# Kernel tuning notes

Measured on AMD Instinct MI355X. Metric: run time of the kernel, lower is better.

Reference implementation:

```python
import jax, jax.numpy as jnp
import numpy as np

HID = 64   # RNN_HID_SIZE
FEAT = 9   # feature dim, hard-coded in module
T = 36     # SEQ_LEN


def setup_inputs() -> dict:
    key = jax.random.key(0)
    ks = jax.random.split(key, 20)
    B = 16384

    def u(k, shape, stdv):
        return jax.random.uniform(k, shape, jnp.float32, -stdv, stdv)

    s_h = 1.0 / np.sqrt(HID)    # stdv for layers with 64 rows / fan-in 64
    s_f = 1.0 / np.sqrt(FEAT)   # stdv 1/3 for feature-sized layers
    s_c = 1.0 / np.sqrt(2 * FEAT)  # weight_combine: Linear(18, 9)

    inp = {
        "values": jax.random.normal(ks[0], (B, T, FEAT), jnp.float32),
        "masks": (jax.random.uniform(ks[1], (B, T, FEAT)) < 0.8).astype(jnp.float32),
        "deltas": jax.random.uniform(ks[2], (B, T, FEAT), jnp.float32, 0.0, 5.0),
        # TemporalDecay h: W [64, 9], stdv = 1/sqrt(64)
        "W_gh": u(ks[3], (HID, FEAT), s_h), "b_gh": u(ks[4], (HID,), s_h),
        # TemporalDecay x (diag): W [9, 9], stdv = 1/sqrt(9)
        "W_gx": u(ks[5], (FEAT, FEAT), s_f), "b_gx": u(ks[6], (FEAT,), s_f),
        # hist_reg: Linear(64, 9)
        "W_hist": u(ks[7], (FEAT, HID), s_h), "b_hist": u(ks[8], (FEAT,), s_h),
        "W_feat": u(ks[9], (FEAT, FEAT), s_f), "b_feat": u(ks[10], (FEAT,), s_f),
        # weight_combine: Linear(18, 9)
        "W_comb": u(ks[11], (FEAT, 2 * FEAT), s_c), "b_comb": u(ks[12], (FEAT,), s_c),
        # LSTMCell(18, 64): gates order i, f, g, o
        "W_ih": u(ks[13], (4 * HID, 2 * FEAT), s_h), "W_hh": u(ks[14], (4 * HID, HID), s_h),
        "b_ih": u(ks[15], (4 * HID,), s_h), "b_hh": u(ks[16], (4 * HID,), s_h),
    }
    return inp


def reference(values, masks, deltas, W_gh, b_gh, W_gx, b_gx, W_hist, b_hist,
              W_feat, b_feat, W_comb, b_comb, W_ih, W_hh, b_ih, b_hh):
    B = values.shape[0]
    dt = values.dtype
    eye = jnp.eye(FEAT, dtype=dt)
    Wgx_diag = W_gx * eye            # TemporalDecay diag mask
    Wfeat_off = W_feat * (1.0 - eye)

    # time-major for scan: [T, B, F]
    xs = (jnp.swapaxes(values, 0, 1), jnp.swapaxes(masks, 0, 1), jnp.swapaxes(deltas, 0, 1))

    def step(carry, xt):
        h, c, loss = carry
        x, m, d = xt
        gamma_h = jnp.exp(-jax.nn.relu(d @ W_gh.T + b_gh))   # [B, 64]
        gamma_x = jnp.exp(-jax.nn.relu(d @ Wgx_diag.T + b_gx))  # [B, 9]
        h = h * gamma_h
        x_h = h @ W_hist.T + b_hist
        denom = jnp.sum(m) + 1e-5
        x_c = m * x + (1.0 - m) * x_h
        z_h = x_c @ Wfeat_off.T + b_feat
        alpha = jnp.concatenate([gamma_x, m], axis=1) @ W_comb.T + b_comb
        c_h = alpha * z_h + (1.0 - alpha) * x_h
        loss = loss + (jnp.sum(jnp.abs(x - x_h) * m)
                       + jnp.sum(jnp.abs(x - z_h) * m)
                       + jnp.sum(jnp.abs(x - c_h) * m)) / denom
        c_c = m * x + (1.0 - m) * c_h
        inp = jnp.concatenate([c_c, m], axis=1)              # [B, 18]
        gates = inp @ W_ih.T + b_ih + h @ W_hh.T + b_hh      # [B, 256]
        i, f, g, o = jnp.split(gates, 4, axis=1)
        c = jax.nn.sigmoid(f) * c + jax.nn.sigmoid(i) * jnp.tanh(g)
        h = jax.nn.sigmoid(o) * jnp.tanh(c)
        return (h, c, loss), c_c

    init = (jnp.zeros((B, HID), dt), jnp.zeros((B, HID), dt), jnp.zeros((), dt))
    (_, _, loss), imps = jax.lax.scan(step, init, xs)
    imputations = jnp.swapaxes(imps, 0, 1)  # [B, T, F]
    return loss / T, imputations
```

## Files before the change

### kernel.cpp

```cpp
#include <hip/hip_runtime.h>

typedef _Float16 hh;
typedef _Float16 h2  __attribute__((ext_vector_type(2)));
typedef _Float16 v4h __attribute__((ext_vector_type(4)));
typedef _Float16 v8h __attribute__((ext_vector_type(8)));
typedef float v4f    __attribute__((ext_vector_type(4)));
typedef unsigned short u16;

#define T_STEPS 36
#define FEAT 9
#define HID 64
#define BT 32
#define SIN_STR 232
#define PK_STR 40

__device__ __forceinline__ float fast_exp2(float x) {
#if __has_builtin(__builtin_amdgcn_exp2f)
  return __builtin_amdgcn_exp2f(x);
#else
  return exp2f(x);
#endif
}
__device__ __forceinline__ float fast_rcp(float x) {
#if __has_builtin(__builtin_amdgcn_rcpf)
  return __builtin_amdgcn_rcpf(x);
#else
  return 1.f / x;
#endif
}
__device__ __forceinline__ float sigmoid_fast(float x) {
  return fast_rcp(1.f + fast_exp2(x * -1.442695041f));
}
__device__ __forceinline__ float tanh_fast(float x) {
  return 1.f - 2.f * fast_rcp(1.f + fast_exp2(x * 2.885390082f));
}
__device__ __forceinline__ float fdot2(h2 a, h2 b, float c) {
#if __has_builtin(__builtin_amdgcn_fdot2)
  return __builtin_amdgcn_fdot2(a, b, c, false);
#else
  return c + (float)a[0] * (float)b[0] + (float)a[1] * (float)b[1];
#endif
}
__device__ __forceinline__ h2 mkh2(hh a, hh b) { h2 r; r[0] = a; r[1] = b; return r; }
__device__ __forceinline__ v4f mfma16(v8h a, v8h b, v4f c) {
  return __builtin_amdgcn_mfma_f32_16x16x32_f16(a, b, c, 0, 0, 0);
}

__global__ void zero_ws(float* __restrict__ ws, float* __restrict__ out) {
  int tid = threadIdx.x;
  if (tid < T_STEPS) ws[tid] = 0.f;
  if (tid == 0) out[0] = 0.f;
}

__global__ __launch_bounds__(256) void denom_kernel(const float* __restrict__ masks,
                                                    float* __restrict__ ws) {
  __shared__ float red[T_STEPS];
  const int tid = threadIdx.x;
  const int e = blockIdx.x * 256 + tid;
  if (tid < T_STEPS) red[tid] = 0.f;
  float acc[T_STEPS];
#pragma unroll
  for (int t = 0; t < T_STEPS; ++t) acc[t] = 0.f;
  const float4* p = (const float4*)masks + (size_t)e * 81;
#pragma unroll
  for (int c = 0; c < 81; ++c) {
    float4 v = p[c];
    acc[(4 * c) / 9]     += v.x;
    acc[(4 * c + 1) / 9] += v.y;
    acc[(4 * c + 2) / 9] += v.z;
    acc[(4 * c + 3) / 9] += v.w;
  }
  __syncthreads();
  int rot = tid % T_STEPS;
#pragma unroll
  for (int t = 0; t < T_STEPS; ++t) {
    int tt = rot + t; if (tt >= T_STEPS) tt -= T_STEPS;
    atomicAdd(&red[tt], acc[tt]);
  }
  __syncthreads();
  if (tid < T_STEPS) atomicAdd(&ws[tid], red[tid]);
}


__global__ __launch_bounds__(256, 2) void rits_kernel(
    const float* __restrict__ values, const float* __restrict__ masks,
    const float* __restrict__ deltas,
    const float* __restrict__ W_gh, const float* __restrict__ b_gh,
    const float* __restrict__ W_gx, const float* __restrict__ b_gx,
    const float* __restrict__ W_hist, const float* __restrict__ b_hist,
    const float* __restrict__ W_feat, const float* __restrict__ b_feat,
    const float* __restrict__ W_comb, const float* __restrict__ b_comb,
    const float* __restrict__ W_ih, const float* __restrict__ W_hh,
    const float* __restrict__ b_ih, const float* __restrict__ b_hh,
    const float* __restrict__ denom, float* __restrict__ out) {

  __shared__ __align__(16) hh sIn[BT * SIN_STR];
  __shared__ __align__(16) hh sPk[BT * PK_STR];
  __shared__ float sRed[256];

  const int tid = threadIdx.x;
  const int lane = tid & 63;
  const int wid = tid >> 6;
  const int q = lane >> 4;
  const int nlo = lane & 15;
  const int b0 = blockIdx.x * BT;
  const int j_col = 16 * wid + nlo;

  v8h bG[4][3];
#pragma unroll
  for (int p = 0; p < 4; ++p)
#pragma unroll
    for (int kt = 0; kt < 3; ++kt) {
      int n = 64 * p + j_col;
      v8h r;
#pragma unroll
      for (int jj = 0; jj < 8; ++jj) {
        int k = kt * 32 + q * 8 + jj;
        float v = 0.f;
        if (k < 18)       v = W_ih[n * 18 + k];
        else if (k < 82)  v = W_hh[n * 64 + (k - 18)];
        else if (k == 82) v = b_ih[n] + b_hh[n];
        r[jj] = (hh)v;
      }
      bG[p][kt] = r;
    }
  v8h bH[3];
#pragma unroll
  for (int kt = 0; kt < 3; ++kt) {
    v8h r;
#pragma unroll
    for (int jj = 0; jj < 8; ++jj) {
      int k = kt * 32 + q * 8 + jj;
      float v = 0.f;
      if (nlo < 9) {
        if (k >= 18 && k < 82) v = W_hist[nlo * 64 + (k - 18)];
        else if (k == 82)      v = b_hist[nlo];
      }
      r[jj] = (hh)v;
    }
    bH[kt] = r;
  }
  v8h bGamA, bGamB;
  {
    int n = j_col;
    v8h ra, rb;
#pragma unroll
    for (int jj = 0; jj < 8; ++jj) {
      int k = q * 8 + jj;
      float va = 0.f, vb = 0.f;
      if (k == 2) va = b_gh[n];
      else if (k >= 16 && k < 25) va = W_gh[n * 9 + (k - 16)];
      if (k >= 2 && k < 11) vb = W_gh[n * 9 + (k - 2)];
      else if (k == 12) vb = b_gh[n];
      ra[jj] = (hh)va; rb[jj] = (hh)vb;
    }
    bGamA = ra; bGamB = rb;
  }

  const int eP = tid >> 3, fqw = tid & 7;
  h2 wf1[5], wf2[5], wc1[9], wc2[9];
  float bf1 = b_feat[fqw], bf2 = b_feat[8];
  float bc1v = b_comb[fqw], bc2v = b_comb[8];
#pragma unroll
  for (int j = 0; j < 5; ++j) {
    int i0 = 2 * j, i1 = 2 * j + 1;
    hh a0 = (hh)((i0 == fqw) ? 0.f : W_feat[fqw * 9 + i0]);
    hh a1 = (hh)((i1 < 9) ? ((i1 == fqw) ? 0.f : W_feat[fqw * 9 + i1]) : 0.f);
    wf1[j] = mkh2(a0, a1);
    hh c0 = (hh)((i0 == 8) ? 0.f : W_feat[8 * 9 + i0]);
    hh c1 = (hh)((i1 < 9) ? W_feat[8 * 9 + i1] : 0.f);
    wf2[j] = mkh2(c0, c1);
  }
#pragma unroll
  for (int j = 0; j < 9; ++j) {
    wc1[j] = mkh2((hh)W_comb[fqw * 18 + 2 * j], (hh)W_comb[fqw * 18 + 2 * j + 1]);
    wc2[j] = mkh2((hh)W_comb[8 * 18 + 2 * j], (hh)W_comb[8 * 18 + 2 * j + 1]);
  }
  float wgx[9], bgxv[9];
#pragma unroll
  for (int f = 0; f < 9; ++f) { wgx[f] = W_gx[f * 9 + f]; bgxv[f] = b_gx[f]; }

  for (int i = tid; i < BT * SIN_STR; i += 256) sIn[i] = (hh)0.f;
  __syncthreads();
  if (tid < BT) {
    sIn[tid * SIN_STR + 82] = (hh)1.f;
    sIn[tid * SIN_STR + 178] = (hh)1.f;
    sIn[tid * SIN_STR + 212] = (hh)1.f;
  }
  const int e1 = tid / 9, f1 = tid - 9 * e1;
  const int e2g = (tid + 256) / 9, f2g = (tid + 256) - 9 * e2g;
  float dreg0 = 0.f, dreg1 = 0.f;
  {
    size_t off = (size_t)(b0 + e1) * (T_STEPS * FEAT) + f1;
    sPk[e1 * PK_STR + f1] = (hh)values[off];
    sPk[e1 * PK_STR + 9 + f1] = (hh)masks[off];
    sPk[e1 * PK_STR + 27 + f1] = (hh)deltas[off];
    float d1 = deltas[off + FEAT];
    dreg0 = d1;
    sIn[e1 * SIN_STR + 202 + f1] = (hh)d1;
    if (tid < 32) {
      size_t off2 = (size_t)(b0 + e2g) * (T_STEPS * FEAT) + f2g;
      sPk[e2g * PK_STR + f2g] = (hh)values[off2];
      sPk[e2g * PK_STR + 9 + f2g] = (hh)masks[off2];
      sPk[e2g * PK_STR + 27 + f2g] = (hh)deltas[off2];
      float d1b = deltas[off2 + FEAT];
      dreg1 = d1b;
      sIn[e2g * SIN_STR + 202 + f2g] = (hh)d1b;
    }
  }
  __syncthreads();

  float c_s[8];
#pragma unroll
  for (int i = 0; i < 8; ++i) c_s[i] = 0.f;
  float loss_acc = 0.f;

  for (int t = 0; t < T_STEPS; ++t) {
    const float inv_den = fast_rcp(denom[t] + 1e-5f);

    v4f gacc[2];
    {
      const int sel = (t + 1) & 1;
      const int awin = 176 + sel * 24;
#pragma unroll
      for (int mt = 0; mt < 2; ++mt) {
        v8h a = *(const v8h*)&sIn[(mt * 16 + nlo) * SIN_STR + awin + q * 8];
        v4f z4 = {0.f, 0.f, 0.f, 0.f};
        gacc[mt] = sel ? mfma16(a, bGamB, z4) : mfma16(a, bGamA, z4);
      }
    }
    if (wid < 2) {
      const int base = (t & 1) * 96;
      v4f acc = {0.f, 0.f, 0.f, 0.f};
#pragma unroll
      for (int kt = 0; kt < 3; ++kt) {
        v8h a = *(const v8h*)&sIn[(wid * 16 + nlo) * SIN_STR + base + kt * 32 + q * 8];
        acc = mfma16(a, bH[kt], acc);
      }
      if (nlo < 9) {
#pragma unroll
        for (int r = 0; r < 4; ++r)
          sPk[(wid * 16 + q * 4 + r) * PK_STR + 18 + nlo] = (hh)acc[r];
      }
    }
    __syncthreads();

    {
      const int pk = eP * PK_STR;
      float x_f  = (float)sPk[pk + fqw];
      float m_f  = (float)sPk[pk + 9 + fqw];
      float xh_f = (float)sPk[pk + 18 + fqw];
      v8h r0 = *(const v8h*)&sPk[pk];
      v8h r1 = *(const v8h*)&sPk[pk + 8];
      v8h r2 = *(const v8h*)&sPk[pk + 16];
      v8h r3 = *(const v8h*)&sPk[pk + 24];
      v4h r4 = *(const v4h*)&sPk[pk + 32];
      hh xxh[9] = {r0[0],r0[1],r0[2],r0[3],r0[4],r0[5],r0[6],r0[7],r1[0]};
      hh mmh[9] = {r1[1],r1[2],r1[3],r1[4],r1[5],r1[6],r1[7],r2[0],r2[1]};
      hh xhh[9] = {r2[2],r2[3],r2[4],r2[5],r2[6],r2[7],r3[0],r3[1],r3[2]};
      hh ddh[9] = {r3[3],r3[4],r3[5],r3[6],r3[7],r4[0],r4[1],r4[2],r4[3]};
      hh xch[10];
#pragma unroll
      for (int f = 0; f < 9; ++f) {
        u16 mb = __builtin_bit_cast(u16, mmh[f]);
        xch[f] = mb ? xxh[f] : xhh[f];
      }
      xch[9] = (hh)0.f;
      hh gxh[9];
#pragma unroll
      for (int f = 0; f < 9; ++f) {
        float y = fmaxf((float)ddh[f] * wgx[f] + bgxv[f], 0.f);
        gxh[f] = (hh)fast_exp2(y * -1.442695041f);
      }
      h2 xc2[5] = {mkh2(xch[0],xch[1]), mkh2(xch[2],xch[3]), mkh2(xch[4],xch[5]),
                   mkh2(xch[6],xch[7]), mkh2(xch[8],xch[9])};
      h2 g2[9]  = {mkh2(gxh[0],gxh[1]), mkh2(gxh[2],gxh[3]), mkh2(gxh[4],gxh[5]),
                   mkh2(gxh[6],gxh[7]), mkh2(gxh[8],mmh[0]), mkh2(mmh[1],mmh[2]),
                   mkh2(mmh[3],mmh[4]), mkh2(mmh[5],mmh[6]), mkh2(mmh[7],mmh[8])};
      float z1 = bf1, a1 = bc1v;
#pragma unroll
      for (int j = 0; j < 5; ++j) z1 = fdot2(wf1[j], xc2[j], z1);
#pragma unroll
      for (int j = 0; j < 9; ++j) a1 = fdot2(wc1[j], g2[j], a1);
      float ch1 = xh_f + a1 * (z1 - xh_f);
      bool obs1 = (m_f != 0.f);
      float cc1 = obs1 ? x_f : ch1;
      float lterm = obs1 ? (fabsf(x_f - xh_f) + fabsf(x_f - z1) + fabsf(x_f - ch1)) : 0.f;
      const int pb = (t & 1) * 96;
      sIn[eP * SIN_STR + pb + fqw] = (hh)cc1;
      sIn[eP * SIN_STR + pb + 9 + fqw] = (hh)m_f;
      out[1 + (size_t)(b0 + eP) * (T_STEPS * FEAT) + t * FEAT + fqw] = cc1;
      if (fqw == 7) {
        float z2 = bf2, a2 = bc2v;
#pragma unroll
        for (int j = 0; j < 5; ++j) z2 = fdot2(wf2[j], xc2[j], z2);
#pragma unroll
        for (int j = 0; j < 9; ++j) a2 = fdot2(wc2[j], g2[j], a2);
        float x8 = (float)xxh[8], m8 = (float)mmh[8], xh8 = (float)xhh[8];
        float ch2 = xh8 + a2 * (z2 - xh8);
        bool obs2 = (m8 != 0.f);
        float cc2 = obs2 ? x8 : ch2;
        lterm += obs2 ? (fabsf(x8 - xh8) + fabsf(x8 - z2) + fabsf(x8 - ch2)) : 0.f;
        sIn[eP * SIN_STR + pb + 8] = (hh)cc2;
        sIn[eP * SIN_STR + pb + 17] = mmh[8];
        out[1 + (size_t)(b0 + eP) * (T_STEPS * FEAT) + t * FEAT + 8] = cc2;
      }
      loss_acc += lterm * inv_den;
    }
    __syncthreads();

    {
      float px0 = 0.f, pm0 = 0.f, px1 = 0.f, pm1 = 0.f, pd0 = 0.f, pd1 = 0.f;
      const bool pre1 = (t + 1 < T_STEPS), pre2 = (t + 2 < T_STEPS);
      if (pre1) {
        size_t off = (size_t)(b0 + e1) * (T_STEPS * FEAT) + (t + 1) * FEAT + f1;
        px0 = values[off]; pm0 = masks[off];
        if (tid < 32) {
          size_t off2 = (size_t)(b0 + e2g) * (T_STEPS * FEAT) + (t + 1) * FEAT + f2g;
          px1 = values[off2]; pm1 = masks[off2];
        }
      }
      if (pre2) {
        size_t offd = (size_t)(b0 + e1) * (T_STEPS * FEAT) + (t + 2) * FEAT + f1;
        pd0 = deltas[offd];
        if (tid < 32) {
          size_t offd2 = (size_t)(b0 + e2g) * (T_STEPS * FEAT) + (t + 2) * FEAT + f2g;
          pd1 = deltas[offd2];
        }
      }

      const int base = (t & 1) * 96;
      const int pub = ((t + 1) & 1) * 96;
      v8h af[2][3];
#pragma unroll
      for (int mt = 0; mt < 2; ++mt)
#pragma unroll
        for (int kt = 0; kt < 3; ++kt)
          af[mt][kt] = *(const v8h*)&sIn[(mt * 16 + nlo) * SIN_STR + base + kt * 32 + q * 8];

      v4f acc[2][4];
#pragma unroll
      for (int mt = 0; mt < 2; ++mt)
#pragma unroll
        for (int p = 0; p < 4; ++p)
          acc[mt][p] = (v4f){0.f, 0.f, 0.f, 0.f};
#pragma unroll
      for (int mt = 0; mt < 2; ++mt)
#pragma unroll
        for (int p = 0; p < 4; ++p)
#pragma unroll
          for (int kt = 0; kt < 3; ++kt)
            acc[mt][p] = mfma16(af[mt][kt], bG[p][kt], acc[mt][p]);

#pragma unroll
      for (int mt = 0; mt < 2; ++mt) {
#pragma unroll
        for (int r = 0; r < 4; ++r) {
          float ig = sigmoid_fast(acc[mt][0][r]);
          float fg = sigmoid_fast(acc[mt][1][r]);
          float gg = tanh_fast(acc[mt][2][r]);
          float og = sigmoid_fast(acc[mt][3][r]);
          float cn = fg * c_s[mt * 4 + r] + ig * gg;
          c_s[mt * 4 + r] = cn;
          float hn = og * tanh_fast(cn);
          float gam = fast_exp2(fmaxf(gacc[mt][r], 0.f) * -1.442695041f);
          sIn[(mt * 16 + q * 4 + r) * SIN_STR + pub + 18 + j_col] = (hh)(hn * gam);
        }
      }

      if (pre1) {
        sPk[e1 * PK_STR + f1] = (hh)px0;
        sPk[e1 * PK_STR + 9 + f1] = (hh)pm0;
        sPk[e1 * PK_STR + 27 + f1] = (hh)dreg0;
        if (tid < 32) {
          sPk[e2g * PK_STR + f2g] = (hh)px1;
          sPk[e2g * PK_STR + 9 + f2g] = (hh)pm1;
          sPk[e2g * PK_STR + 27 + f2g] = (hh)dreg1;
        }
      }
      if (pre2) {
        const int sb = 192 + (t & 1) * 10;
        sIn[e1 * SIN_STR + sb + f1] = (hh)pd0;
        dreg0 = pd0;
        if (tid < 32) { sIn[e2g * SIN_STR + sb + f2g] = (hh)pd1; dreg1 = pd1; }
      }
    }
    __syncthreads();
  }

  sRed[tid] = loss_acc;
  __syncthreads();
  for (int k = 128; k > 0; k >>= 1) {
    if (tid < k) sRed[tid] += sRed[tid + k];
    __syncthreads();
  }
  if (tid == 0) atomicAdd(out, sRed[0] * (1.f / (float)T_STEPS));
}

extern "C" void kernel_launch(void* const* d_in, const int* in_sizes, int n_in,
                              void* d_out, int out_size, void* d_ws, size_t ws_size,
                              hipStream_t stream) {
  const float* values = (const float*)d_in[0];
  const float* masks  = (const float*)d_in[1];
  const float* deltas = (const float*)d_in[2];
  const float* W_gh   = (const float*)d_in[3];
  const float* b_gh   = (const float*)d_in[4];
  const float* W_gx   = (const float*)d_in[5];
  const float* b_gx   = (const float*)d_in[6];
  const float* W_hist = (const float*)d_in[7];
  const float* b_hist = (const float*)d_in[8];
  const float* W_feat = (const float*)d_in[9];
  const float* b_feat = (const float*)d_in[10];
  const float* W_comb = (const float*)d_in[11];
  const float* b_comb = (const float*)d_in[12];
  const float* W_ih   = (const float*)d_in[13];
  const float* W_hh   = (const float*)d_in[14];
  const float* b_ih   = (const float*)d_in[15];
  const float* b_hh   = (const float*)d_in[16];

  float* out = (float*)d_out;
  float* ws  = (float*)d_ws;
  int B = in_sizes[0] / (T_STEPS * FEAT);

  zero_ws<<<1, 64, 0, stream>>>(ws, out);
  denom_kernel<<<B / 256, 256, 0, stream>>>(masks, ws);
  rits_kernel<<<B / BT, 256, 0, stream>>>(values, masks, deltas,
                                          W_gh, b_gh, W_gx, b_gx,
                                          W_hist, b_hist, W_feat, b_feat,
                                          W_comb, b_comb, W_ih, W_hh,
                                          b_ih, b_hh, ws, out);
}
```

Baseline: 284.4 us.

## Halve batch tile per block to raise occupancy and re-split mask denominator reduction

After: 496.2 us. 74.5% more time.

```diff
diff --git a/kernel.cpp b/kernel.cpp
--- a/kernel.cpp
+++ b/kernel.cpp
@@ -10,7 +10,7 @@
 #define T_STEPS 36
 #define FEAT 9
 #define HID 64
-#define BT 32
+#define BT 16
 #define SIN_STR 232
 #define PK_STR 40
 
@@ -56,33 +56,27 @@
                                                     float* __restrict__ ws) {
   __shared__ float red[T_STEPS];
   const int tid = threadIdx.x;
-  const int e = blockIdx.x * 256 + tid;
   if (tid < T_STEPS) red[tid] = 0.f;
-  float acc[T_STEPS];
-#pragma unroll
-  for (int t = 0; t < T_STEPS; ++t) acc[t] = 0.f;
-  const float4* p = (const float4*)masks + (size_t)e * 81;
-#pragma unroll
-  for (int c = 0; c < 81; ++c) {
+  __syncthreads();
+  const int idx = blockIdx.x * 256 + tid;
+  const int t0 = (idx % 9) * 4;
+  const float4* p = (const float4*)masks + (size_t)idx * 9;
+  float acc[4] = {0.f, 0.f, 0.f, 0.f};
+#pragma unroll
+  for (int c = 0; c < 9; ++c) {
     float4 v = p[c];
     acc[(4 * c) / 9]     += v.x;
     acc[(4 * c + 1) / 9] += v.y;
     acc[(4 * c + 2) / 9] += v.z;
     acc[(4 * c + 3) / 9] += v.w;
   }
-  __syncthreads();
-  int rot = tid % T_STEPS;
-#pragma unroll
-  for (int t = 0; t < T_STEPS; ++t) {
-    int tt = rot + t; if (tt >= T_STEPS) tt -= T_STEPS;
-    atomicAdd(&red[tt], acc[tt]);
-  }
+#pragma unroll
+  for (int j = 0; j < 4; ++j) atomicAdd(&red[t0 + j], acc[j]);
   __syncthreads();
   if (tid < T_STEPS) atomicAdd(&ws[tid], red[tid]);
 }
 
-
-__global__ __launch_bounds__(256, 2) void rits_kernel(
+__global__ __launch_bounds__(256, 4) void rits_kernel(
     const float* __restrict__ values, const float* __restrict__ masks,
     const float* __restrict__ deltas,
     const float* __restrict__ W_gh, const float* __restrict__ b_gh,
@@ -188,9 +182,9 @@
     sIn[tid * SIN_STR + 212] = (hh)1.f;
   }
   const int e1 = tid / 9, f1 = tid - 9 * e1;
-  const int e2g = (tid + 256) / 9, f2g = (tid + 256) - 9 * e2g;
-  float dreg0 = 0.f, dreg1 = 0.f;
-  {
+  const bool ldr = (tid < 9 * BT);
+  float dreg0 = 0.f;
+  if (ldr) {
     size_t off = (size_t)(b0 + e1) * (T_STEPS * FEAT) + f1;
     sPk[e1 * PK_STR + f1] = (hh)values[off];
     sPk[e1 * PK_STR + 9 + f1] = (hh)masks[off];
@@ -198,54 +192,42 @@
     float d1 = deltas[off + FEAT];
     dreg0 = d1;
     sIn[e1 * SIN_STR + 202 + f1] = (hh)d1;
-    if (tid < 32) {
-      size_t off2 = (size_t)(b0 + e2g) * (T_STEPS * FEAT) + f2g;
-      sPk[e2g * PK_STR + f2g] = (hh)values[off2];
-      sPk[e2g * PK_STR + 9 + f2g] = (hh)masks[off2];
-      sPk[e2g * PK_STR + 27 + f2g] = (hh)deltas[off2];
-      float d1b = deltas[off2 + FEAT];
-      dreg1 = d1b;
-      sIn[e2g * SIN_STR + 202 + f2g] = (hh)d1b;
-    }
-  }
-  __syncthreads();
-
-  float c_s[8];
-#pragma unroll
-  for (int i = 0; i < 8; ++i) c_s[i] = 0.f;
+  }
+  __syncthreads();
+
+  float c_s[4];
+#pragma unroll
+  for (int i = 0; i < 4; ++i) c_s[i] = 0.f;
   float loss_acc = 0.f;
 
   for (int t = 0; t < T_STEPS; ++t) {
     const float inv_den = fast_rcp(denom[t] + 1e-5f);
 
-    v4f gacc[2];
+    v4f gacc;
     {
       const int sel = (t + 1) & 1;
       const int awin = 176 + sel * 24;
-#pragma unroll
-      for (int mt = 0; mt < 2; ++mt) {
-        v8h a = *(const v8h*)&sIn[(mt * 16 + nlo) * SIN_STR + awin + q * 8];
-        v4f z4 = {0.f, 0.f, 0.f, 0.f};
-        gacc[mt] = sel ? mfma16(a, bGamB, z4) : mfma16(a, bGamA, z4);
-      }
-    }
-    if (wid < 2) {
+      v8h a = *(const v8h*)&sIn[nlo * SIN_STR + awin + q * 8];
+      v4f z4 = {0.f, 0.f, 0.f, 0.f};
+      gacc = sel ? mfma16(a, bGamB, z4) : mfma16(a, bGamA, z4);
+    }
+    if (wid == 0) {
       const int base = (t & 1) * 96;
       v4f acc = {0.f, 0.f, 0.f, 0.f};
 #pragma unroll
       for (int kt = 0; kt < 3; ++kt) {
-        v8h a = *(const v8h*)&sIn[(wid * 16 + nlo) * SIN_STR + base + kt * 32 + q * 8];
+        v8h a = *(const v8h*)&sIn[nlo * SIN_STR + base + kt * 32 + q * 8];
         acc = mfma16(a, bH[kt], acc);
       }
       if (nlo < 9) {
 #pragma unroll
         for (int r = 0; r < 4; ++r)
-          sPk[(wid * 16 + q * 4 + r) * PK_STR + 18 + nlo] = (hh)acc[r];
+          sPk[(q * 4 + r) * PK_STR + 18 + nlo] = (hh)acc[r];
       }
     }
     __syncthreads();
 
-    {
+    if (eP < BT) {
       const int pk = eP * PK_STR;
       float x_f  = (float)sPk[pk + fqw];
       float m_f  = (float)sPk[pk + 9 + fqw];
@@ -310,79 +292,57 @@
     __syncthreads();
 
     {
-      float px0 = 0.f, pm0 = 0.f, px1 = 0.f, pm1 = 0.f, pd0 = 0.f, pd1 = 0.f;
-      const bool pre1 = (t + 1 < T_STEPS), pre2 = (t + 2 < T_STEPS);
+      float px0 = 0.f, pm0 = 0.f, pd0 = 0.f;
+      const bool pre1 = ldr && (t + 1 < T_STEPS);
+      const bool pre2 = ldr && (t + 2 < T_STEPS);
       if (pre1) {
         size_t off = (size_t)(b0 + e1) * (T_STEPS * FEAT) + (t + 1) * FEAT + f1;
         px0 = values[off]; pm0 = masks[off];
-        if (tid < 32) {
-          size_t off2 = (size_t)(b0 + e2g) * (T_STEPS * FEAT) + (t + 1) * FEAT + f2g;
-          px1 = values[off2]; pm1 = masks[off2];
-        }
       }
       if (pre2) {
         size_t offd = (size_t)(b0 + e1) * (T_STEPS * FEAT) + (t + 2) * FEAT + f1;
         pd0 = deltas[offd];
-        if (tid < 32) {
-          size_t offd2 = (size_t)(b0 + e2g) * (T_STEPS * FEAT) + (t + 2) * FEAT + f2g;
-          pd1 = deltas[offd2];
-        }
       }
 
       const int base = (t & 1) * 96;
       const int pub = ((t + 1) & 1) * 96;
-      v8h af[2][3];
-#pragma unroll
-      for (int mt = 0; mt < 2; ++mt)
+      v8h af[3];
+#pragma unroll
+      for (int kt = 0; kt < 3; ++kt)
+        af[kt] = *(const v8h*)&sIn[nlo * SIN_STR + base + kt * 32 + q * 8];
+
+      v4f acc[4];
+#pragma unroll
+      for (int p = 0; p < 4; ++p)
+        acc[p] = (v4f){0.f, 0.f, 0.f, 0.f};
+#pragma unroll
+      for (int p = 0; p < 4; ++p)
 #pragma unroll
         for (int kt = 0; kt < 3; ++kt)
-          af[mt][kt] = *(const v8h*)&sIn[(mt * 16 + nlo) * SIN_STR + base + kt * 32 + q * 8];
-
-      v4f acc[2][4];
-#pragma unroll
-      for (int mt = 0; mt < 2; ++mt)
-#pragma unroll
-        for (int p = 0; p < 4; ++p)
-          acc[mt][p] = (v4f){0.f, 0.f, 0.f, 0.f};
-#pragma unroll
-      for (int mt = 0; mt < 2; ++mt)
-#pragma unroll
-        for (int p = 0; p < 4; ++p)
-#pragma unroll
-          for (int kt = 0; kt < 3; ++kt)
-            acc[mt][p] = mfma16(af[mt][kt], bG[p][kt], acc[mt][p]);
-
-#pragma unroll
-      for (int mt = 0; mt < 2; ++mt) {
-#pragma unroll
-        for (int r = 0; r < 4; ++r) {
-          float ig = sigmoid_fast(acc[mt][0][r]);
-          float fg = sigmoid_fast(acc[mt][1][r]);
-          float gg = tanh_fast(acc[mt][2][r]);
-          float og = sigmoid_fast(acc[mt][3][r]);
-          float cn = fg * c_s[mt * 4 + r] + ig * gg;
-          c_s[mt * 4 + r] = cn;
-          float hn = og * tanh_fast(cn);
-          float gam = fast_exp2(fmaxf(gacc[mt][r], 0.f) * -1.442695041f);
-          sIn[(mt * 16 + q * 4 + r) * SIN_STR + pub + 18 + j_col] = (hh)(hn * gam);
-        }
+          acc[p] = mfma16(af[kt], bG[p][kt], acc[p]);
+
+#pragma unroll
+      for (int r = 0; r < 4; ++r) {
+        float ig = sigmoid_fast(acc[0][r]);
+        float fg = sigmoid_fast(acc[1][r]);
+        float gg = tanh_fast(acc[2][r]);
+        float og = sigmoid_fast(acc[3][r]);
+        float cn = fg * c_s[r] + ig * gg;
+        c_s[r] = cn;
+        float hn = og * tanh_fast(cn);
+        float gam = fast_exp2(fmaxf(gacc[r], 0.f) * -1.442695041f);
+        sIn[(q * 4 + r) * SIN_STR + pub + 18 + j_col] = (hh)(hn * gam);
       }
 
       if (pre1) {
         sPk[e1 * PK_STR + f1] = (hh)px0;
         sPk[e1 * PK_STR + 9 + f1] = (hh)pm0;
         sPk[e1 * PK_STR + 27 + f1] = (hh)dreg0;
-        if (tid < 32) {
-          sPk[e2g * PK_STR + f2g] = (hh)px1;
-          sPk[e2g * PK_STR + 9 + f2g] = (hh)pm1;
-          sPk[e2g * PK_STR + 27 + f2g] = (hh)dreg1;
-        }
       }
       if (pre2) {
         const int sb = 192 + (t & 1) * 10;
         sIn[e1 * SIN_STR + sb + f1] = (hh)pd0;
         dreg0 = pd0;
-        if (tid < 32) { sIn[e2g * SIN_STR + sb + f2g] = (hh)pd1; dreg1 = pd1; }
       }
     }
     __syncthreads();
@@ -423,7 +383,7 @@
   int B = in_sizes[0] / (T_STEPS * FEAT);
 
   zero_ws<<<1, 64, 0, stream>>>(ws, out);
-  denom_kernel<<<B / 256, 256, 0, stream>>>(masks, ws);
+  denom_kernel<<<(B * 9) / 256, 256, 0, stream>>>(masks, ws);
   rits_kernel<<<B / BT, 256, 0, stream>>>(values, masks, deltas,
                                           W_gh, b_gh, W_gx, b_gx,
                                           W_hist, b_hist, W_feat, b_feat,
```
